# Kernel optimization log

Hardware: AMD Instinct MI355X
Metric: run time of the kernel (lower is better)

Reference implementation:

```python
import jax, jax.numpy as jnp
import numpy as np

TOP_K = 4  # num_experts_per_tok

def _silu(x):
    return x * jax.nn.sigmoid(x)

def setup_inputs() -> dict:
    key = jax.random.key(0)
    ks = jax.random.split(key, 6)
    T, H, E, I, S = 1024, 2048, 16, 1408, 2  # tokens, hidden, experts, moe_intermediate, shared experts
    scale = 0.02
    return {
        "hidden_states": jax.random.normal(ks[0], (T, H), jnp.float32),
        "gate_w": jax.random.normal(ks[1], (E, H), jnp.float32) * scale,          # router weight [E, H]
        "w_gate_up": jax.random.normal(ks[2], (E, 2 * I, H), jnp.float32) * scale,  # merged gate+up per expert
        "w_down": jax.random.normal(ks[3], (E, H, I), jnp.float32) * scale,
        "shared_gate_up": jax.random.normal(ks[4], (2 * I * S, H), jnp.float32) * scale,
        "shared_down": jax.random.normal(ks[5], (H, I * S), jnp.float32) * scale,
    }

def reference(hidden_states, gate_w, w_gate_up, w_down, shared_gate_up, shared_down):
    x = hidden_states  # [T, H]
    T, H = x.shape
    E = gate_w.shape[0]

    # ---- shared experts (BailingMLP, SiluAndMul) ----
    gu_s = x @ shared_gate_up.T                      # [T, 2*I*S]
    g_s, u_s = jnp.split(gu_s, 2, axis=-1)
    shared_out = (_silu(g_s) * u_s) @ shared_down.T  # [T, H]

    # ---- router: fp32 linear, softmax score, top-k, renormalize ----
    logits = (x.astype(jnp.float32) @ gate_w.astype(jnp.float32).T).astype(x.dtype)  # [T, E]
    probs = jax.nn.softmax(logits.astype(jnp.float32), axis=-1)
    topk_w, topk_idx = jax.lax.top_k(probs, TOP_K)                 # [T, K]
    topk_w = topk_w / jnp.sum(topk_w, axis=-1, keepdims=True)      # norm_topk_prob=True
    # routed_scaling_factor = 1.0 (no-op)
    combine = jnp.zeros((T, E), jnp.float32).at[jnp.arange(T)[:, None], topk_idx].add(topk_w)
    combine = combine.astype(x.dtype)                              # [T, E] sparse combine weights

    # ---- routed experts: dense per-expert SiLU-gated MLP, weighted combine ----
    gu = jnp.einsum('th,eih->tei', x, w_gate_up)     # [T, E, 2I]
    g_e, u_e = jnp.split(gu, 2, axis=-1)
    act = _silu(g_e) * u_e                           # [T, E, I]
    down = jnp.einsum('tei,ehi->teh', act, w_down)   # [T, E, H]
    routed = jnp.einsum('teh,te->th', down, combine) # [T, H]

    return routed + shared_out
```

## Files before the change

### kernel.cpp

```cpp
#include <hip/hip_runtime.h>
#include <stdint.h>

#define T_TOK 1024
#define H_DIM 2048
#define E_NUM 16
#define I_DIM 1408
#define IS_DIM 2816
#define TOPK 4

#define BK 32
#define LDP 40

typedef unsigned short u16;
typedef __bf16 bf16x8 __attribute__((ext_vector_type(8)));
typedef float f32x4 __attribute__((ext_vector_type(4)));

__device__ __forceinline__ u16 f2bf(float f) {
  unsigned int v; __builtin_memcpy(&v, &f, 4);
  unsigned int lsb = (v >> 16) & 1u;
  v += 0x7fffu + lsb;
  return (u16)(v >> 16);
}

__device__ __forceinline__ uint2 cvt4(float4 v) {
  uint2 o;
  o.x = (unsigned)f2bf(v.x) | ((unsigned)f2bf(v.y) << 16);
  o.y = (unsigned)f2bf(v.z) | ((unsigned)f2bf(v.w) << 16);
  return o;
}

__device__ __forceinline__ f32x4 mfma16(bf16x8 a, bf16x8 b, f32x4 c) {
  return __builtin_amdgcn_mfma_f32_16x16x32_bf16(a, b, c, 0, 0, 0);
}

__global__ __launch_bounds__(256) void router_kernel(
    const float* __restrict__ x, const float* __restrict__ gw,
    float* __restrict__ combine, int* __restrict__ topk_idx) {
  __shared__ float partial[256];
  __shared__ float logits[E_NUM];
  const int t = blockIdx.x, tid = threadIdx.x;
  const int e = tid >> 4, l16 = tid & 15;
  const float* xr = x + (size_t)t * H_DIM;
  const float* wr = gw + (size_t)e * H_DIM;
  float s = 0.f;
  for (int h = l16 * 4; h < H_DIM; h += 64) {
    float4 xv = *(const float4*)&xr[h];
    float4 wv = *(const float4*)&wr[h];
    s += xv.x * wv.x + xv.y * wv.y + xv.z * wv.z + xv.w * wv.w;
  }
  partial[tid] = s;
  __syncthreads();
  if (tid < E_NUM) {
    float tot = 0.f;
    for (int j = 0; j < 16; ++j) tot += partial[tid * 16 + j];
    logits[tid] = tot;
  }
  __syncthreads();
  if (tid == 0) {
    float p[E_NUM];
    float mx = -1e30f;
    for (int i = 0; i < E_NUM; ++i) mx = fmaxf(mx, logits[i]);
    float sum = 0.f;
    for (int i = 0; i < E_NUM; ++i) { p[i] = expf(logits[i] - mx); sum += p[i]; }
    float inv = 1.f / sum;
    for (int i = 0; i < E_NUM; ++i) p[i] *= inv;
    bool used[E_NUM];
    for (int i = 0; i < E_NUM; ++i) used[i] = false;
    int idx[TOPK]; float w4[TOPK]; float wsum = 0.f;
    for (int k = 0; k < TOPK; ++k) {
      int best = 0; float bv = -1.f;
      for (int i = 0; i < E_NUM; ++i)
        if (!used[i] && p[i] > bv) { bv = p[i]; best = i; }
      used[best] = true; idx[k] = best; w4[k] = bv; wsum += bv;
    }
    float outw[E_NUM];
    for (int i = 0; i < E_NUM; ++i) outw[i] = 0.f;
    float winv = 1.f / wsum;
    for (int k = 0; k < TOPK; ++k) {
      outw[idx[k]] = w4[k] * winv;
      topk_idx[t * TOPK + k] = idx[k];
    }
    for (int i = 0; i < E_NUM; ++i) combine[(size_t)t * E_NUM + i] = outw[i];
  }
}

__global__ __launch_bounds__(256) void assign_kernel(
    const int* __restrict__ topk_idx, int* __restrict__ list,
    int* __restrict__ cnt, int* __restrict__ cntPad) {
  __shared__ int lcnt[E_NUM], lcur[E_NUM];
  const int tid = threadIdx.x;
  if (tid < E_NUM) { lcnt[tid] = 0; lcur[tid] = 0; }
  __syncthreads();
  for (int t = tid; t < T_TOK; t += 256)
    for (int k = 0; k < TOPK; ++k)
      atomicAdd(&lcnt[topk_idx[t * TOPK + k]], 1);
  __syncthreads();
  for (int t = tid; t < T_TOK; t += 256)
    for (int k = 0; k < TOPK; ++k) {
      int e = topk_idx[t * TOPK + k];
      int p = atomicAdd(&lcur[e], 1);
      list[e * T_TOK + p] = t;
    }
  __syncthreads();
  if (tid < E_NUM) {
    int c = lcnt[tid];
    int cp = (c + 127) / 128 * 128;
    cnt[tid] = c;
    cntPad[tid] = cp;
    int last = (c > 0) ? list[tid * T_TOK + c - 1] : 0;
    for (int p = c; p < cp; ++p) list[tid * T_TOK + p] = last;
  }
}

__global__ __launch_bounds__(256, 2) void gateup_kernel(
    const float* __restrict__ X, const float* __restrict__ Wgu,
    const float* __restrict__ Wsh, const float* __restrict__ combine,
    const int* __restrict__ list, const int* __restrict__ cntPad,
    u16* __restrict__ actR, u16* __restrict__ actS) {
  __shared__ u16 As[128 * LDP];
  __shared__ u16 Wg[64 * LDP];
  __shared__ u16 Wu[64 * LDP];
  __shared__ int ltok[128];
  const int z = blockIdx.z;
  const int row0 = blockIdx.y * 128;
  const int tid = threadIdx.x;
  const int srow = tid >> 3;
  const int scol = (tid & 7) * 4;

  const float* Arow[4];
  const float* Wgp;
  const float* Wup;
  int n0;
  if (z >= E_NUM) {
    n0 = (blockIdx.x + (z - E_NUM) * 22) * 64;
    Wgp = Wsh + (size_t)(n0 + srow) * H_DIM + scol;
    Wup = Wsh + (size_t)(IS_DIM + n0 + srow) * H_DIM + scol;
#pragma unroll
    for (int q = 0; q < 4; ++q)
      Arow[q] = X + (size_t)(row0 + q * 32 + srow) * H_DIM + scol;
  } else {
    if (row0 >= cntPad[z]) return;
    if (tid < 128) ltok[tid] = list[z * T_TOK + row0 + tid];
    __syncthreads();
    n0 = blockIdx.x * 64;
    Wgp = Wgu + (size_t)z * (2 * I_DIM * H_DIM) + (size_t)(n0 + srow) * H_DIM + scol;
    Wup = Wgp + (size_t)I_DIM * H_DIM;
#pragma unroll
    for (int q = 0; q < 4; ++q)
      Arow[q] = X + (size_t)ltok[q * 32 + srow] * H_DIM + scol;
  }

  const int wave = tid >> 6, lane = tid & 63;
  const int lane16 = lane & 15, quad = lane >> 4;
  const int wm = wave >> 1, wn = wave & 1;

  const f32x4 zero = {0.f, 0.f, 0.f, 0.f};
  f32x4 accg[4][2], accu[4][2];
#pragma unroll
  for (int i = 0; i < 4; ++i)
#pragma unroll
    for (int j = 0; j < 2; ++j) { accg[i][j] = zero; accu[i][j] = zero; }

  float4 pa0, pa1, pa2, pa3, pg0, pg1, pu0, pu1;
#define GU_LOAD(k0)                                 \
  pa0 = *(const float4*)(Arow[0] + (k0));           \
  pa1 = *(const float4*)(Arow[1] + (k0));           \
  pa2 = *(const float4*)(Arow[2] + (k0));           \
  pa3 = *(const float4*)(Arow[3] + (k0));           \
  pg0 = *(const float4*)(Wgp + (k0));               \
  pg1 = *(const float4*)(Wgp + 32 * H_DIM + (k0));  \
  pu0 = *(const float4*)(Wup + (k0));               \
  pu1 = *(const float4*)(Wup + 32 * H_DIM + (k0));

  GU_LOAD(0)
  for (int k0 = 0; k0 < H_DIM; k0 += BK) {
    *(uint2*)&As[srow * LDP + scol]        = cvt4(pa0);
    *(uint2*)&As[(32 + srow) * LDP + scol] = cvt4(pa1);
    *(uint2*)&As[(64 + srow) * LDP + scol] = cvt4(pa2);
    *(uint2*)&As[(96 + srow) * LDP + scol] = cvt4(pa3);
    *(uint2*)&Wg[srow * LDP + scol]        = cvt4(pg0);
    *(uint2*)&Wg[(32 + srow) * LDP + scol] = cvt4(pg1);
    *(uint2*)&Wu[srow * LDP + scol]        = cvt4(pu0);
    *(uint2*)&Wu[(32 + srow) * LDP + scol] = cvt4(pu1);
    __syncthreads();
    if (k0 + BK < H_DIM) { GU_LOAD(k0 + BK) }
    bf16x8 a[4], bg[2], bu[2];
#pragma unroll
    for (int i = 0; i < 4; ++i)
      a[i] = *(const bf16x8*)&As[(wm * 64 + i * 16 + lane16) * LDP + quad * 8];
#pragma unroll
    for (int j = 0; j < 2; ++j) {
      bg[j] = *(const bf16x8*)&Wg[(wn * 32 + j * 16 + lane16) * LDP + quad * 8];
      bu[j] = *(const bf16x8*)&Wu[(wn * 32 + j * 16 + lane16) * LDP + quad * 8];
    }
#pragma unroll
    for (int i = 0; i < 4; ++i)
#pragma unroll
      for (int j = 0; j < 2; ++j) {
        accg[i][j] = mfma16(a[i], bg[j], accg[i][j]);
        accu[i][j] = mfma16(a[i], bu[j], accu[i][j]);
      }
    __syncthreads();
  }
#undef GU_LOAD

  if (z >= E_NUM) {
#pragma unroll
    for (int i = 0; i < 4; ++i)
#pragma unroll
      for (int j = 0; j < 2; ++j) {
        const int col = n0 + wn * 32 + j * 16 + lane16;
#pragma unroll
        for (int r = 0; r < 4; ++r) {
          const int row = row0 + wm * 64 + i * 16 + quad * 4 + r;
          float g = accg[i][j][r], u = accu[i][j][r];
          actS[(size_t)row * IS_DIM + col] = f2bf(g / (1.f + __expf(-g)) * u);
        }
      }
  } else {
#pragma unroll
    for (int i = 0; i < 4; ++i)
#pragma unroll
      for (int j = 0; j < 2; ++j) {
        const int col = n0 + wn * 32 + j * 16 + lane16;
#pragma unroll
        for (int r = 0; r < 4; ++r) {
          const int rl = wm * 64 + i * 16 + quad * 4 + r;
          float g = accg[i][j][r], u = accu[i][j][r];
          float act = g / (1.f + __expf(-g)) * u;
          act *= combine[(size_t)ltok[rl] * E_NUM + z];
          actR[((size_t)z * T_TOK + row0 + rl) * I_DIM + col] = f2bf(act);
        }
      }
  }
}

__global__ __launch_bounds__(256, 2) void down_kernel(
    const u16* __restrict__ actR, const u16* __restrict__ actS,
    const float* __restrict__ Wd, const float* __restrict__ Wsd,
    const int* __restrict__ list, const int* __restrict__ cnt,
    const int* __restrict__ cntPad, float* __restrict__ out) {
  __shared__ u16 As[128 * LDP];
  __shared__ u16 Bs[128 * LDP];
  __shared__ int ltok[128];
  const int z = blockIdx.z;
  const int row0 = blockIdx.y * 128;
  const int col0 = blockIdx.x * 128;
  const int tid = threadIdx.x;
  const int arow = tid >> 2, acol = (tid & 3) * 8;
  const int brow = tid >> 3, bcol = (tid & 7) * 4;

  int K, c = 0;
  const u16* Ap;
  const float* Bp;
  if (z == E_NUM) {
    K = IS_DIM;
    Ap = actS + (size_t)(row0 + arow) * IS_DIM + acol;
    Bp = Wsd + (size_t)(col0 + brow) * IS_DIM + bcol;
  } else {
    if (row0 >= cntPad[z]) return;
    if (tid < 128) ltok[tid] = list[z * T_TOK + row0 + tid];
    c = cnt[z];
    K = I_DIM;
    Ap = actR + ((size_t)z * T_TOK + row0 + arow) * I_DIM + acol;
    Bp = Wd + ((size_t)z * H_DIM + col0 + brow) * I_DIM + bcol;
  }
  const u16* Ap1 = Ap + (size_t)64 * K;
  const float* Bp1 = Bp + (size_t)32 * K;
  const float* Bp2 = Bp + (size_t)64 * K;
  const float* Bp3 = Bp + (size_t)96 * K;

  const int wave = tid >> 6, lane = tid & 63;
  const int lane16 = lane & 15, quad = lane >> 4;
  const int wm = wave >> 1, wn = wave & 1;

  const f32x4 zero = {0.f, 0.f, 0.f, 0.f};
  f32x4 acc[4][4];
#pragma unroll
  for (int i = 0; i < 4; ++i)
#pragma unroll
    for (int j = 0; j < 4; ++j) acc[i][j] = zero;

  uint4 qa0, qa1; float4 pb0, pb1, pb2, pb3;
#define DN_LOAD(k0)                        \
  qa0 = *(const uint4*)(Ap + (k0));        \
  qa1 = *(const uint4*)(Ap1 + (k0));       \
  pb0 = *(const float4*)(Bp + (k0));       \
  pb1 = *(const float4*)(Bp1 + (k0));      \
  pb2 = *(const float4*)(Bp2 + (k0));      \
  pb3 = *(const float4*)(Bp3 + (k0));

  DN_LOAD(0)
  for (int k0 = 0; k0 < K; k0 += BK) {
    *(uint4*)&As[arow * LDP + acol]        = qa0;
    *(uint4*)&As[(64 + arow) * LDP + acol] = qa1;
    *(uint2*)&Bs[brow * LDP + bcol]        = cvt4(pb0);
    *(uint2*)&Bs[(32 + brow) * LDP + bcol] = cvt4(pb1);
    *(uint2*)&Bs[(64 + brow) * LDP + bcol] = cvt4(pb2);
    *(uint2*)&Bs[(96 + brow) * LDP + bcol] = cvt4(pb3);
    __syncthreads();
    if (k0 + BK < K) { DN_LOAD(k0 + BK) }
    bf16x8 a[4], b[4];
#pragma unroll
    for (int i = 0; i < 4; ++i)
      a[i] = *(const bf16x8*)&As[(wm * 64 + i * 16 + lane16) * LDP + quad * 8];
#pragma unroll
    for (int j = 0; j < 4; ++j)
      b[j] = *(const bf16x8*)&Bs[(wn * 64 + j * 16 + lane16) * LDP + quad * 8];
#pragma unroll
    for (int i = 0; i < 4; ++i)
#pragma unroll
      for (int j = 0; j < 4; ++j) acc[i][j] = mfma16(a[i], b[j], acc[i][j]);
    __syncthreads();
  }
#undef DN_LOAD

  if (z == E_NUM) {
#pragma unroll
    for (int i = 0; i < 4; ++i)
#pragma unroll
      for (int j = 0; j < 4; ++j) {
        const int col = col0 + wn * 64 + j * 16 + lane16;
#pragma unroll
        for (int r = 0; r < 4; ++r) {
          const int row = row0 + wm * 64 + i * 16 + quad * 4 + r;
          atomicAdd(&out[(size_t)row * H_DIM + col], acc[i][j][r]);
        }
      }
  } else {
#pragma unroll
    for (int i = 0; i < 4; ++i)
#pragma unroll
      for (int j = 0; j < 4; ++j) {
        const int col = col0 + wn * 64 + j * 16 + lane16;
#pragma unroll
        for (int r = 0; r < 4; ++r) {
          const int rl = wm * 64 + i * 16 + quad * 4 + r;
          if (row0 + rl < c)
            atomicAdd(&out[(size_t)ltok[rl] * H_DIM + col], acc[i][j][r]);
        }
      }
  }
}

extern "C" void kernel_launch(void* const* d_in, const int* in_sizes, int n_in,
                              void* d_out, int out_size, void* d_ws,
                              size_t ws_size, hipStream_t stream) {
  const float* x = (const float*)d_in[0];
  const float* gate_w = (const float*)d_in[1];
  const float* w_gate_up = (const float*)d_in[2];
  const float* w_down = (const float*)d_in[3];
  const float* shared_gu = (const float*)d_in[4];
  const float* shared_down = (const float*)d_in[5];
  float* out = (float*)d_out;

  char* ws = (char*)d_ws;
  float* combine = (float*)ws;
  int* topk_idx = (int*)(ws + 65536);
  int* list = (int*)(ws + 81920);
  int* cnt = (int*)(ws + 147456);
  int* cntPad = (int*)(ws + 147520);
  u16* actS = (u16*)(ws + 147584);
  u16* actR = (u16*)(ws + 147584 + 5767168);

  router_kernel<<<T_TOK, 256, 0, stream>>>(x, gate_w, combine, topk_idx);
  assign_kernel<<<1, 256, 0, stream>>>(topk_idx, list, cnt, cntPad);
  hipMemsetAsync(out, 0, (size_t)T_TOK * H_DIM * sizeof(float), stream);

  gateup_kernel<<<dim3(22, 8, 18), 256, 0, stream>>>(
      x, w_gate_up, shared_gu, combine, list, cntPad, actR, actS);

  down_kernel<<<dim3(16, 8, 17), 256, 0, stream>>>(
      actR, actS, w_down, shared_down, list, cnt, cntPad, out);
}
```

Before: 909.5 us.

## Pre-convert activations to bf16 in router, compact expert buffers, swap grid order

```diff
diff --git a/kernel.cpp b/kernel.cpp
--- a/kernel.cpp
+++ b/kernel.cpp
@@ -13,20 +13,19 @@
 
 typedef unsigned short u16;
 typedef __bf16 bf16x8 __attribute__((ext_vector_type(8)));
+typedef __bf16 bf16x4v __attribute__((ext_vector_type(4)));
 typedef float f32x4 __attribute__((ext_vector_type(4)));
 
 __device__ __forceinline__ u16 f2bf(float f) {
-  unsigned int v; __builtin_memcpy(&v, &f, 4);
-  unsigned int lsb = (v >> 16) & 1u;
-  v += 0x7fffu + lsb;
-  return (u16)(v >> 16);
+  __bf16 h = (__bf16)f;
+  u16 r; __builtin_memcpy(&r, &h, 2); return r;
 }
 
 __device__ __forceinline__ uint2 cvt4(float4 v) {
-  uint2 o;
-  o.x = (unsigned)f2bf(v.x) | ((unsigned)f2bf(v.y) << 16);
-  o.y = (unsigned)f2bf(v.z) | ((unsigned)f2bf(v.w) << 16);
-  return o;
+  bf16x4v h;
+  h[0] = (__bf16)v.x; h[1] = (__bf16)v.y;
+  h[2] = (__bf16)v.z; h[3] = (__bf16)v.w;
+  uint2 o; __builtin_memcpy(&o, &h, 8); return o;
 }
 
 __device__ __forceinline__ f32x4 mfma16(bf16x8 a, bf16x8 b, f32x4 c) {
@@ -35,7 +34,8 @@
 
 __global__ __launch_bounds__(256) void router_kernel(
     const float* __restrict__ x, const float* __restrict__ gw,
-    float* __restrict__ combine, int* __restrict__ topk_idx) {
+    float* __restrict__ combine, int* __restrict__ topk_idx,
+    u16* __restrict__ xb) {
   __shared__ float partial[256];
   __shared__ float logits[E_NUM];
   const int t = blockIdx.x, tid = threadIdx.x;
@@ -49,6 +49,14 @@
     s += xv.x * wv.x + xv.y * wv.y + xv.z * wv.z + xv.w * wv.w;
   }
   partial[tid] = s;
+  {
+    const int h0 = tid * 8;
+    float4 v0 = *(const float4*)&xr[h0];
+    float4 v1 = *(const float4*)&xr[h0 + 4];
+    uint2 a = cvt4(v0), b = cvt4(v1);
+    uint4 o; o.x = a.x; o.y = a.y; o.z = b.x; o.w = b.y;
+    *(uint4*)&xb[(size_t)t * H_DIM + h0] = o;
+  }
   __syncthreads();
   if (tid < E_NUM) {
     float tot = 0.f;
@@ -86,8 +94,8 @@
 
 __global__ __launch_bounds__(256) void assign_kernel(
     const int* __restrict__ topk_idx, int* __restrict__ list,
-    int* __restrict__ cnt, int* __restrict__ cntPad) {
-  __shared__ int lcnt[E_NUM], lcur[E_NUM];
+    int* __restrict__ cnt, int* __restrict__ cntPad, int* __restrict__ base) {
+  __shared__ int lcnt[E_NUM], lcur[E_NUM], lpad[E_NUM];
   const int tid = threadIdx.x;
   if (tid < E_NUM) { lcnt[tid] = 0; lcur[tid] = 0; }
   __syncthreads();
@@ -107,47 +115,53 @@
     int cp = (c + 127) / 128 * 128;
     cnt[tid] = c;
     cntPad[tid] = cp;
+    lpad[tid] = cp;
     int last = (c > 0) ? list[tid * T_TOK + c - 1] : 0;
     for (int p = c; p < cp; ++p) list[tid * T_TOK + p] = last;
   }
+  __syncthreads();
+  if (tid == 0) {
+    int b = 0;
+    for (int e2 = 0; e2 < E_NUM; ++e2) { base[e2] = b; b += lpad[e2]; }
+  }
 }
 
 __global__ __launch_bounds__(256, 2) void gateup_kernel(
-    const float* __restrict__ X, const float* __restrict__ Wgu,
+    const u16* __restrict__ Xb, const float* __restrict__ Wgu,
     const float* __restrict__ Wsh, const float* __restrict__ combine,
     const int* __restrict__ list, const int* __restrict__ cntPad,
-    u16* __restrict__ actR, u16* __restrict__ actS) {
+    const int* __restrict__ base, u16* __restrict__ actR,
+    u16* __restrict__ actS) {
   __shared__ u16 As[128 * LDP];
   __shared__ u16 Wg[64 * LDP];
   __shared__ u16 Wu[64 * LDP];
   __shared__ int ltok[128];
   const int z = blockIdx.z;
-  const int row0 = blockIdx.y * 128;
+  const int row0 = blockIdx.x * 128;
   const int tid = threadIdx.x;
-  const int srow = tid >> 3;
-  const int scol = (tid & 7) * 4;
-
-  const float* Arow[4];
-  const float* Wgp;
-  const float* Wup;
+  const int srow = tid >> 3, scol = (tid & 7) * 4;
+  const int srowA = tid >> 2, scolA = (tid & 3) * 8;
+
+  const u16 *Aq0, *Aq1;
+  const float *Wgp, *Wup;
   int n0;
+  size_t outRow0 = 0;
   if (z >= E_NUM) {
-    n0 = (blockIdx.x + (z - E_NUM) * 22) * 64;
+    n0 = (blockIdx.y + (z - E_NUM) * 22) * 64;
     Wgp = Wsh + (size_t)(n0 + srow) * H_DIM + scol;
     Wup = Wsh + (size_t)(IS_DIM + n0 + srow) * H_DIM + scol;
-#pragma unroll
-    for (int q = 0; q < 4; ++q)
-      Arow[q] = X + (size_t)(row0 + q * 32 + srow) * H_DIM + scol;
+    Aq0 = Xb + (size_t)(row0 + srowA) * H_DIM + scolA;
+    Aq1 = Xb + (size_t)(row0 + 64 + srowA) * H_DIM + scolA;
   } else {
     if (row0 >= cntPad[z]) return;
     if (tid < 128) ltok[tid] = list[z * T_TOK + row0 + tid];
     __syncthreads();
-    n0 = blockIdx.x * 64;
+    n0 = blockIdx.y * 64;
     Wgp = Wgu + (size_t)z * (2 * I_DIM * H_DIM) + (size_t)(n0 + srow) * H_DIM + scol;
     Wup = Wgp + (size_t)I_DIM * H_DIM;
-#pragma unroll
-    for (int q = 0; q < 4; ++q)
-      Arow[q] = X + (size_t)ltok[q * 32 + srow] * H_DIM + scol;
+    Aq0 = Xb + (size_t)ltok[srowA] * H_DIM + scolA;
+    Aq1 = Xb + (size_t)ltok[64 + srowA] * H_DIM + scolA;
+    outRow0 = (size_t)(base[z] + row0);
   }
 
   const int wave = tid >> 6, lane = tid & 63;
@@ -161,12 +175,10 @@
 #pragma unroll
     for (int j = 0; j < 2; ++j) { accg[i][j] = zero; accu[i][j] = zero; }
 
-  float4 pa0, pa1, pa2, pa3, pg0, pg1, pu0, pu1;
+  uint4 pa0, pa1; float4 pg0, pg1, pu0, pu1;
 #define GU_LOAD(k0)                                 \
-  pa0 = *(const float4*)(Arow[0] + (k0));           \
-  pa1 = *(const float4*)(Arow[1] + (k0));           \
-  pa2 = *(const float4*)(Arow[2] + (k0));           \
-  pa3 = *(const float4*)(Arow[3] + (k0));           \
+  pa0 = *(const uint4*)(Aq0 + (k0));                \
+  pa1 = *(const uint4*)(Aq1 + (k0));                \
   pg0 = *(const float4*)(Wgp + (k0));               \
   pg1 = *(const float4*)(Wgp + 32 * H_DIM + (k0));  \
   pu0 = *(const float4*)(Wup + (k0));               \
@@ -174,14 +186,12 @@
 
   GU_LOAD(0)
   for (int k0 = 0; k0 < H_DIM; k0 += BK) {
-    *(uint2*)&As[srow * LDP + scol]        = cvt4(pa0);
-    *(uint2*)&As[(32 + srow) * LDP + scol] = cvt4(pa1);
-    *(uint2*)&As[(64 + srow) * LDP + scol] = cvt4(pa2);
-    *(uint2*)&As[(96 + srow) * LDP + scol] = cvt4(pa3);
-    *(uint2*)&Wg[srow * LDP + scol]        = cvt4(pg0);
-    *(uint2*)&Wg[(32 + srow) * LDP + scol] = cvt4(pg1);
-    *(uint2*)&Wu[srow * LDP + scol]        = cvt4(pu0);
-    *(uint2*)&Wu[(32 + srow) * LDP + scol] = cvt4(pu1);
+    *(uint4*)&As[srowA * LDP + scolA]        = pa0;
+    *(uint4*)&As[(64 + srowA) * LDP + scolA] = pa1;
+    *(uint2*)&Wg[srow * LDP + scol]          = cvt4(pg0);
+    *(uint2*)&Wg[(32 + srow) * LDP + scol]   = cvt4(pg1);
+    *(uint2*)&Wu[srow * LDP + scol]          = cvt4(pu0);
+    *(uint2*)&Wu[(32 + srow) * LDP + scol]   = cvt4(pu1);
     __syncthreads();
     if (k0 + BK < H_DIM) { GU_LOAD(k0 + BK) }
     bf16x8 a[4], bg[2], bu[2];
@@ -229,7 +239,7 @@
           float g = accg[i][j][r], u = accu[i][j][r];
           float act = g / (1.f + __expf(-g)) * u;
           act *= combine[(size_t)ltok[rl] * E_NUM + z];
-          actR[((size_t)z * T_TOK + row0 + rl) * I_DIM + col] = f2bf(act);
+          actR[(outRow0 + rl) * I_DIM + col] = f2bf(act);
         }
       }
   }
@@ -239,13 +249,14 @@
     const u16* __restrict__ actR, const u16* __restrict__ actS,
     const float* __restrict__ Wd, const float* __restrict__ Wsd,
     const int* __restrict__ list, const int* __restrict__ cnt,
-    const int* __restrict__ cntPad, float* __restrict__ out) {
+    const int* __restrict__ cntPad, const int* __restrict__ base,
+    float* __restrict__ out) {
   __shared__ u16 As[128 * LDP];
   __shared__ u16 Bs[128 * LDP];
   __shared__ int ltok[128];
   const int z = blockIdx.z;
-  const int row0 = blockIdx.y * 128;
-  const int col0 = blockIdx.x * 128;
+  const int row0 = blockIdx.x * 128;
+  const int col0 = blockIdx.y * 128;
   const int tid = threadIdx.x;
   const int arow = tid >> 2, acol = (tid & 3) * 8;
   const int brow = tid >> 3, bcol = (tid & 7) * 4;
@@ -262,7 +273,7 @@
     if (tid < 128) ltok[tid] = list[z * T_TOK + row0 + tid];
     c = cnt[z];
     K = I_DIM;
-    Ap = actR + ((size_t)z * T_TOK + row0 + arow) * I_DIM + acol;
+    Ap = actR + ((size_t)base[z] + row0 + arow) * I_DIM + acol;
     Bp = Wd + ((size_t)z * H_DIM + col0 + brow) * I_DIM + bcol;
   }
   const u16* Ap1 = Ap + (size_t)64 * K;
@@ -360,16 +371,18 @@
   int* list = (int*)(ws + 81920);
   int* cnt = (int*)(ws + 147456);
   int* cntPad = (int*)(ws + 147520);
-  u16* actS = (u16*)(ws + 147584);
-  u16* actR = (u16*)(ws + 147584 + 5767168);
-
-  router_kernel<<<T_TOK, 256, 0, stream>>>(x, gate_w, combine, topk_idx);
-  assign_kernel<<<1, 256, 0, stream>>>(topk_idx, list, cnt, cntPad);
+  int* base = (int*)(ws + 147584);
+  u16* xb = (u16*)(ws + 147648);
+  u16* actS = (u16*)(ws + 147648 + 4194304);
+  u16* actR = (u16*)(ws + 147648 + 4194304 + 5767168);
+
+  router_kernel<<<T_TOK, 256, 0, stream>>>(x, gate_w, combine, topk_idx, xb);
+  assign_kernel<<<1, 256, 0, stream>>>(topk_idx, list, cnt, cntPad, base);
   hipMemsetAsync(out, 0, (size_t)T_TOK * H_DIM * sizeof(float), stream);
 
-  gateup_kernel<<<dim3(22, 8, 18), 256, 0, stream>>>(
-      x, w_gate_up, shared_gu, combine, list, cntPad, actR, actS);
-
-  down_kernel<<<dim3(16, 8, 17), 256, 0, stream>>>(
-      actR, actS, w_down, shared_down, list, cnt, cntPad, out);
-}
+  gateup_kernel<<<dim3(8, 22, 18), 256, 0, stream>>>(
+      xb, w_gate_up, shared_gu, combine, list, cntPad, base, actR, actS);
+
+  down_kernel<<<dim3(8, 16, 17), 256, 0, stream>>>(
+      actR, actS, w_down, shared_down, list, cnt, cntPad, base, out);
+}
```

Result: slower. 1.167 ms (+28.3%).
